# Kernel tuning notes

Measured on AMD Instinct MI355X. Metric: run time of the kernel, lower is better.

## Reference

```python
import jax, jax.numpy as jnp
import numpy as np

NUM_GRAPHS = 256
T, F_IN, F_OUT, D_E = 5, 75, 15, 50   # towers, per-tower in, per-tower out, edge emb dim
N_LAYERS = 4
AVG_DEG_LOG = float(np.log(17.0))     # from deg histogram: all nodes have degree 16 -> mean log(deg+1)=log(17)
BN_EPS = 1e-5
STD_EPS = 1e-5


def _pna_conv(h, src, dst, e_enc, pw, pb, qw, qb, lw, lb):
    """One PNAConv layer (divide_input=False, pre_layers=post_layers=1)."""
    N = h.shape[0]
    x_i, x_j = h[dst], h[src]                      # gather target/source node feats [E, F_IN]
    # pre-NN Linear(3*F_IN -> F_IN) per tower, applied to cat([x_i, x_j, e_enc]); split the weight
    Wi, Wj, We = pw[:, :F_IN], pw[:, F_IN:2 * F_IN], pw[:, 2 * F_IN:]
    m = (jnp.einsum('ef,tfg->etg', x_i, Wi)
         + jnp.einsum('ef,tfg->etg', x_j, Wj)
         + jnp.einsum('ef,tfg->etg', e_enc, We) + pb)   # [E, T, F_IN]
    ones = jnp.ones((m.shape[0],), h.dtype)
    cnt = jax.ops.segment_sum(ones, dst, N)        # in-degree per node
    deg = jnp.maximum(cnt, 1.0)[:, None, None]
    mean = jax.ops.segment_sum(m, dst, N) / deg
    mean2 = jax.ops.segment_sum(m * m, dst, N) / deg
    std = jnp.sqrt(jax.nn.relu(mean2 - mean * mean) + STD_EPS)
    has_edge = (cnt > 0)[:, None, None]
    mn = jnp.where(has_edge, jax.ops.segment_min(m, dst, N), 0.0)
    mx = jnp.where(has_edge, jax.ops.segment_max(m, dst, N), 0.0)
    agg = jnp.concatenate([mean, mn, mx, std], axis=-1)          # [N, T, 4*F_IN]
    amp = (jnp.log(jnp.maximum(cnt, 1.0) + 1.0) / AVG_DEG_LOG)[:, None, None]
    out = jnp.concatenate([agg, agg * amp, agg / amp], axis=-1)  # identity/amplification/attenuation [N,T,12*F_IN]
    post = jnp.einsum('ntf,tfg->ntg', out, qw) + qb              # post-NN Linear(900 -> 15) per tower
    return post.reshape(N, T * F_OUT) @ lw + lb                  # mixing Linear(75 -> 75)


def setup_inputs() -> dict:
    key = jax.random.key(0)
    ks = iter(jax.random.split(key, 64))
    N, E = 16384, 262144
    g = lambda shape, s=0.1: jax.random.normal(next(ks), shape, jnp.float32) * s
    return dict(
        x=jax.random.randint(next(ks), (N,), 0, 21),
        edge_index=jax.random.randint(next(ks), (2, E), 0, N),
        edge_attr=jax.random.randint(next(ks), (E,), 0, 4),
        batch=jnp.sort(jax.random.randint(next(ks), (N,), 0, NUM_GRAPHS)),
        node_emb=g((21, F_IN)),
        edge_emb=g((4, D_E)),
        edge_enc_w=g((N_LAYERS, D_E, F_IN)), edge_enc_b=jnp.zeros((N_LAYERS, F_IN)),
        pre_w=g((N_LAYERS, T, 3 * F_IN, F_IN)), pre_b=jnp.zeros((N_LAYERS, T, F_IN)),
        post_w=g((N_LAYERS, T, 12 * F_IN, F_OUT)), post_b=jnp.zeros((N_LAYERS, T, F_OUT)),
        lin_w=g((N_LAYERS, T * F_OUT, T * F_OUT)), lin_b=jnp.zeros((N_LAYERS, T * F_OUT)),
        bn_gamma=jnp.ones((N_LAYERS, 75)), bn_beta=jnp.zeros((N_LAYERS, 75)),
        mlp_w1=g((75, 50)), mlp_b1=jnp.zeros((50,)),
        mlp_w2=g((50, 25)), mlp_b2=jnp.zeros((25,)),
        mlp_w3=g((25, 1)), mlp_b3=jnp.zeros((1,)),
    )


def reference(x, edge_index, edge_attr, batch, node_emb, edge_emb,
              edge_enc_w, edge_enc_b, pre_w, pre_b, post_w, post_b,
              lin_w, lin_b, bn_gamma, bn_beta,
              mlp_w1, mlp_b1, mlp_w2, mlp_b2, mlp_w3, mlp_b3):
    h = node_emb[x]                    # [N, 75]
    e = edge_emb[edge_attr]            # [E, 50]
    src, dst = edge_index[0], edge_index[1]
    for l in range(N_LAYERS):
        e_enc = e @ edge_enc_w[l] + edge_enc_b[l]   # edge encoder Linear(50->75)
        h = _pna_conv(h, src, dst, e_enc, pre_w[l], pre_b[l],
                      post_w[l], post_b[l], lin_w[l], lin_b[l])
        mu = h.mean(0)
        var = ((h - mu) ** 2).mean(0)               # biased batch-norm variance (training mode)
        h = jax.nn.relu((h - mu) / jnp.sqrt(var + BN_EPS) * bn_gamma[l] + bn_beta[l])
    g = jax.ops.segment_sum(h, batch, NUM_GRAPHS)   # global_add_pool [G, 75]
    g = jax.nn.relu(g @ mlp_w1 + mlp_b1)
    g = jax.nn.relu(g @ mlp_w2 + mlp_b2)
    return g @ mlp_w3 + mlp_b3                      # [G, 1]
```

## Files before the change

### kernel.cpp

```cpp
#include <hip/hip_runtime.h>
#include <math.h>

#define N_NODES 16384
#define N_EDGES 262144
#define TOW 5
#define FI 75
#define FO 15
#define DE 50
#define NL 4
#define NG 256
#define HWP 752
#define AGS 1504
#define PNN 8

static __device__ __attribute__((aligned(16))) float g_hA[N_NODES*FI];
static __device__ __attribute__((aligned(16))) float g_hB[N_NODES*FI];
static __device__ __attribute__((aligned(16))) float g_hW[N_NODES*HWP];
static __device__ __attribute__((aligned(16))) float g_ec[NL*4*376];
static __device__ int   g_deg[N_NODES];
static __device__ int   g_rowstart[N_NODES+1];
static __device__ int   g_cursor[N_NODES];
static __device__ int   g_edge[N_EDGES];
static __device__ float g_mu[FI];
static __device__ float g_rsig[FI];
static __device__ float g_pool[NG*FI];

__global__ void k_embed(const int* __restrict__ x, const float* __restrict__ node_emb) {
    int i = blockIdx.x * blockDim.x + threadIdx.x;
    if (i < N_NODES*FI) {
        int n = i / FI, f = i % FI;
        g_hA[i] = node_emb[x[n]*FI + f];
    }
}

__global__ void k_zerodeg() {
    int i = blockIdx.x * blockDim.x + threadIdx.x;
    if (i < N_NODES) g_deg[i] = 0;
}

__global__ void k_hist(const int* __restrict__ dst) {
    int e = blockIdx.x * blockDim.x + threadIdx.x;
    if (e < N_EDGES) atomicAdd(&g_deg[dst[e]], 1);
}

__global__ void k_scan() {
    __shared__ int part[1024];
    int t = threadIdx.x;
    int base = t * 16;
    int loc[16];
    int s = 0;
    #pragma unroll
    for (int i = 0; i < 16; i++) { loc[i] = s; s += g_deg[base + i]; }
    part[t] = s;
    __syncthreads();
    for (int off = 1; off < 1024; off <<= 1) {
        int v = 0;
        if (t >= off) v = part[t - off];
        __syncthreads();
        if (t >= off) part[t] += v;
        __syncthreads();
    }
    int excl = (t == 0) ? 0 : part[t - 1];
    #pragma unroll
    for (int i = 0; i < 16; i++) {
        g_rowstart[base + i] = excl + loc[i];
        g_cursor[base + i]   = excl + loc[i];
    }
    if (t == 1023) g_rowstart[N_NODES] = part[1023];
}

__global__ void k_scatter(const int* __restrict__ src, const int* __restrict__ dst,
                          const int* __restrict__ attr) {
    int e = blockIdx.x * blockDim.x + threadIdx.x;
    if (e < N_EDGES) {
        int d = dst[e];
        int pos = atomicAdd(&g_cursor[d], 1);
        g_edge[pos] = src[e] | (attr[e] << 16);
    }
}

__global__ void k_ec(const float* __restrict__ edge_emb, const float* __restrict__ edge_enc_w,
                     const float* __restrict__ edge_enc_b, const float* __restrict__ pre_w,
                     const float* __restrict__ pre_b) {
    int l = blockIdx.x;
    const float* eew = edge_enc_w + l*DE*FI;
    const float* eeb = edge_enc_b + l*FI;
    const float* pw  = pre_w + l*TOW*3*FI*FI;
    const float* pb  = pre_b + l*TOW*FI;
    __shared__ float e_enc[4*FI];
    int t = threadIdx.x;
    if (t < 4*FI) {
        int a = t / FI, f = t % FI;
        float s = eeb[f];
        for (int d = 0; d < DE; d++) s += edge_emb[a*DE + d] * eew[d*FI + f];
        e_enc[t] = s;
    }
    __syncthreads();
    for (int o = t; o < 4*376; o += blockDim.x) {
        int a = o / 376;
        int r = o % 376;
        float s = 0.f;
        if (r < TOW*FI) {
            int tw = r / FI, g = r % FI;
            s = pb[tw*FI + g];
            const float* W = pw + (tw*(3*FI) + 2*FI)*FI + g;
            for (int f = 0; f < FI; f++) s += e_enc[a*FI + f] * W[f*FI];
        }
        g_ec[l*1504 + o] = s;
    }
}

#define NPB 8
__global__ void k_hw(const float* __restrict__ pw, const float* __restrict__ gamma,
                     const float* __restrict__ beta, int first) {
    __shared__ float hsh[NPB*FI];
    int n0 = blockIdx.x * NPB;
    int tid = threadIdx.x;
    for (int i = tid; i < NPB*FI; i += blockDim.x) {
        int idx = (n0 + i/FI)*FI + (i % FI);
        float v;
        if (first) {
            v = g_hA[idx];
        } else {
            int c = i % FI;
            v = (g_hB[idx] - g_mu[c]) * g_rsig[c] * gamma[c] + beta[c];
            v = v > 0.f ? v : 0.f;
        }
        hsh[i] = v;
    }
    __syncthreads();
    for (int o = tid; o < 2*TOW*FI; o += blockDim.x) {
        int half = o / (TOW*FI);
        int r = o % (TOW*FI);
        int tw = r / FI, g = r % FI;
        const float* W = pw + (tw*(3*FI) + half*FI)*FI + g;
        float acc[NPB];
        #pragma unroll
        for (int nn = 0; nn < NPB; nn++) acc[nn] = 0.f;
        for (int f = 0; f < FI; f++) {
            float w = W[f*FI];
            #pragma unroll
            for (int nn = 0; nn < NPB; nn++) acc[nn] += hsh[nn*FI + f] * w;
        }
        #pragma unroll
        for (int nn = 0; nn < NPB; nn++)
            g_hW[(n0+nn)*HWP + half*376 + r] = acc[nn];
    }
}

__global__ __launch_bounds__(384) void k_edge(int l, float* __restrict__ agg) {
    __shared__ float aggl[AGS];
    int n = blockIdx.x;
    int tid = threadIdx.x;
    int el = tid & 3;
    int q  = tid >> 2;
    bool act = q < 94;
    const float* ec = g_ec + l*1504;
    int e0 = g_rowstart[n], e1 = g_rowstart[n+1];
    int cnt = e1 - e0;

    if (tid < 4) aggl[1500 + tid] = 0.f;

    float s0=0.f,s1=0.f,s2=0.f,s3=0.f;
    float t0=0.f,t1=0.f,t2=0.f,t3=0.f;
    float mn0=1e30f,mn1=1e30f,mn2=1e30f,mn3=1e30f;
    float mx0=-1e30f,mx1=-1e30f,mx2=-1e30f,mx3=-1e30f;
    float h0=0.f,h1=0.f,h2=0.f,h3=0.f;
    if (act) {
        float4 hv = *(const float4*)&g_hW[n*HWP + 4*q];
        h0=hv.x; h1=hv.y; h2=hv.z; h3=hv.w;
    }

    int nit = (cnt + 15) >> 4;
    for (int it = 0; it < nit; ++it) {
        int ib = e0 + it*16 + el;
        int i0 = ib, i1 = ib+4, i2 = ib+8, i3 = ib+12;
        int pk0 = g_edge[i0 < e1 ? i0 : e0];
        int pk1 = g_edge[i1 < e1 ? i1 : e0];
        int pk2 = g_edge[i2 < e1 ? i2 : e0];
        int pk3 = g_edge[i3 < e1 ? i3 : e0];
        if (act) {
            float4 hj0 = *(const float4*)&g_hW[(pk0 & 0xFFFF)*HWP + 376 + 4*q];
            float4 hj1 = *(const float4*)&g_hW[(pk1 & 0xFFFF)*HWP + 376 + 4*q];
            float4 hj2 = *(const float4*)&g_hW[(pk2 & 0xFFFF)*HWP + 376 + 4*q];
            float4 hj3 = *(const float4*)&g_hW[(pk3 & 0xFFFF)*HWP + 376 + 4*q];
            float4 ev0 = *(const float4*)&ec[(pk0 >> 16)*376 + 4*q];
            float4 ev1 = *(const float4*)&ec[(pk1 >> 16)*376 + 4*q];
            float4 ev2 = *(const float4*)&ec[(pk2 >> 16)*376 + 4*q];
            float4 ev3 = *(const float4*)&ec[(pk3 >> 16)*376 + 4*q];
            #define ACCUM(ii, hj, ev)                                        \
                if (ii < e1) {                                               \
                    float m0 = h0 + hj.x + ev.x;                             \
                    float m1 = h1 + hj.y + ev.y;                             \
                    float m2 = h2 + hj.z + ev.z;                             \
                    float m3 = h3 + hj.w + ev.w;                             \
                    s0 += m0; s1 += m1; s2 += m2; s3 += m3;                  \
                    t0 += m0*m0; t1 += m1*m1; t2 += m2*m2; t3 += m3*m3;      \
                    mn0 = fminf(mn0,m0); mn1 = fminf(mn1,m1);                \
                    mn2 = fminf(mn2,m2); mn3 = fminf(mn3,m3);                \
                    mx0 = fmaxf(mx0,m0); mx1 = fmaxf(mx1,m1);                \
                    mx2 = fmaxf(mx2,m2); mx3 = fmaxf(mx3,m3);                \
                }
            ACCUM(i0, hj0, ev0)
            ACCUM(i1, hj1, ev1)
            ACCUM(i2, hj2, ev2)
            ACCUM(i3, hj3, ev3)
            #undef ACCUM
        }
    }
    #define RSUM(v) v += __shfl_xor(v,1); v += __shfl_xor(v,2);
    #define RMIN(v) v = fminf(v,__shfl_xor(v,1)); v = fminf(v,__shfl_xor(v,2));
    #define RMAX(v) v = fmaxf(v,__shfl_xor(v,1)); v = fmaxf(v,__shfl_xor(v,2));
    RSUM(s0) RSUM(s1) RSUM(s2) RSUM(s3)
    RSUM(t0) RSUM(t1) RSUM(t2) RSUM(t3)
    RMIN(mn0) RMIN(mn1) RMIN(mn2) RMIN(mn3)
    RMAX(mx0) RMAX(mx1) RMAX(mx2) RMAX(mx3)

    if (act && el == 0) {
        float inv = 1.0f / ((cnt > 0) ? (float)cnt : 1.0f);
        float sv[4]  = {s0,s1,s2,s3};
        float tv[4]  = {t0,t1,t2,t3};
        float mnv[4] = {mn0,mn1,mn2,mn3};
        float mxv[4] = {mx0,mx1,mx2,mx3};
        #pragma unroll
        for (int j = 0; j < 4; j++) {
            int c = 4*q + j;
            if (c < TOW*FI) {
                int tw = c / FI, f = c - tw*FI;
                float mean  = sv[j]*inv;
                float mean2 = tv[j]*inv;
                float var = mean2 - mean*mean;
                if (var < 0.f) var = 0.f;
                int b = tw*300 + f;
                aggl[b      ] = mean;
                aggl[b +  75] = (cnt > 0) ? mnv[j] : 0.f;
                aggl[b + 150] = (cnt > 0) ? mxv[j] : 0.f;
                aggl[b + 225] = sqrtf(var + 1e-5f);
            }
        }
    }
    __syncthreads();
    if (tid < 376)
        *(float4*)&agg[(size_t)n*AGS + 4*tid] = *(const float4*)&aggl[4*tid];
}

__global__ __launch_bounds__(384) void
k_post(const float* __restrict__ agg, const float* __restrict__ qw,
       const float* __restrict__ qb, const float* __restrict__ lw,
       const float* __restrict__ lb) {
    __shared__ float part[5*75*9];
    __shared__ float post[PNN][76];
    __shared__ float s_amp[PNN], s_iamp[PNN];
    int tid = threadIdx.x;
    int n0 = blockIdx.x * PNN;

    if (tid < PNN) {
        int cnt = g_rowstart[n0+tid+1] - g_rowstart[n0+tid];
        float deg = (cnt > 0) ? (float)cnt : 1.0f;
        float amp = logf(deg + 1.0f) * (1.0f/2.8332133440562162f);
        s_amp[tid] = amp; s_iamp[tid] = 1.0f/amp;
    }
    __syncthreads();

    int o = tid % 75, p = tid / 75;
    if (tid < 375) {
        int tw = o / FO, g = o % FO;
        const float* W = qw + tw*900*FO + g;
        const float* ab = agg + (size_t)n0*AGS + tw*300 + p*60;
        float a0[PNN], a1[PNN], a2[PNN];
        #pragma unroll
        for (int nn = 0; nn < PNN; nn++) { a0[nn]=0.f; a1[nn]=0.f; a2[nn]=0.f; }
        int f0 = p*60;
        for (int fq = 0; fq < 15; ++fq) {
            int f = f0 + fq*4;
            float w0a = W[(f  )*FO], w0b = W[(f+1)*FO], w0c = W[(f+2)*FO], w0d = W[(f+3)*FO];
            float w1a = W[(300+f)*FO], w1b = W[(301+f)*FO], w1c = W[(302+f)*FO], w1d = W[(303+f)*FO];
            float w2a = W[(600+f)*FO], w2b = W[(601+f)*FO], w2c = W[(602+f)*FO], w2d = W[(603+f)*FO];
            #pragma unroll
            for (int nn = 0; nn < PNN; nn++) {
                float4 av = *(const float4*)&ab[(size_t)nn*AGS + fq*4];
                a0[nn] += av.x*w0a + av.y*w0b + av.z*w0c + av.w*w0d;
                a1[nn] += av.x*w1a + av.y*w1b + av.z*w1c + av.w*w1d;
                a2[nn] += av.x*w2a + av.y*w2b + av.z*w2c + av.w*w2d;
            }
        }
        #pragma unroll
        for (int nn = 0; nn < PNN; nn++)
            part[p*675 + o*9 + nn] = a0[nn] + s_amp[nn]*a1[nn] + s_iamp[nn]*a2[nn];
    }
    __syncthreads();
    if (tid < 75) {
        #pragma unroll
        for (int nn = 0; nn < PNN; nn++) {
            float s = qb[tid];
            #pragma unroll
            for (int p2 = 0; p2 < 5; p2++) s += part[p2*675 + tid*9 + nn];
            post[nn][tid] = s;
        }
    }
    __syncthreads();
    if (tid < 300) {
        int oo = tid % 75, nna = tid / 75;
        #pragma unroll
        for (int h = 0; h < 2; ++h) {
            int nn = nna + 4*h;
            const float* Wl = lw + oo;
            float s = lb[oo];
            for (int f = 0; f < 75; f++) s += post[nn][f] * Wl[f*75];
            g_hB[(n0+nn)*FI + oo] = s;
        }
    }
}

__global__ void k_bnstat() {
    int c = blockIdx.x;
    int t = threadIdx.x;
    double s = 0.0, s2 = 0.0;
    for (int n = t; n < N_NODES; n += 256) {
        float v = g_hB[n*FI + c];
        s += v; s2 += (double)v * v;
    }
    __shared__ double ps[256], ps2[256];
    ps[t] = s; ps2[t] = s2;
    __syncthreads();
    for (int off = 128; off > 0; off >>= 1) {
        if (t < off) { ps[t] += ps[t+off]; ps2[t] += ps2[t+off]; }
        __syncthreads();
    }
    if (t == 0) {
        double mu = ps[0] / N_NODES;
        double var = ps2[0] / N_NODES - mu*mu;
        if (var < 0.0) var = 0.0;
        g_mu[c]   = (float)mu;
        g_rsig[c] = (float)(1.0 / sqrt(var + 1e-5));
    }
}

__global__ void k_poolzero() {
    int i = blockIdx.x * blockDim.x + threadIdx.x;
    if (i < NG*FI) g_pool[i] = 0.f;
}

__global__ void k_pool(const int* __restrict__ batch, const float* __restrict__ gamma,
                       const float* __restrict__ beta) {
    int i = blockIdx.x * blockDim.x + threadIdx.x;
    if (i < N_NODES*FI) {
        int n = i / FI, c = i % FI;
        float v = (g_hB[i] - g_mu[c]) * g_rsig[c] * gamma[c] + beta[c];
        v = v > 0.f ? v : 0.f;
        atomicAdd(&g_pool[batch[n]*FI + c], v);
    }
}

__global__ void k_mlp(const float* __restrict__ w1, const float* __restrict__ b1,
                      const float* __restrict__ w2, const float* __restrict__ b2,
                      const float* __restrict__ w3, const float* __restrict__ b3,
                      float* __restrict__ out) {
    __shared__ float gin[FI], h1[50], h2[25];
    int gi = blockIdx.x;
    int t = threadIdx.x;
    if (t < FI) gin[t] = g_pool[gi*FI + t];
    __syncthreads();
    if (t < 50) {
        float s = b1[t];
        for (int f = 0; f < FI; f++) s += gin[f] * w1[f*50 + t];
        h1[t] = s > 0.f ? s : 0.f;
    }
    __syncthreads();
    if (t < 25) {
        float s = b2[t];
        for (int f = 0; f < 50; f++) s += h1[f] * w2[f*25 + t];
        h2[t] = s > 0.f ? s : 0.f;
    }
    __syncthreads();
    if (t == 0) {
        float s = b3[0];
        for (int f = 0; f < 25; f++) s += h2[f] * w3[f];
        out[gi] = s;
    }
}

extern "C" void kernel_launch(void* const* d_in, const int* in_sizes, int n_in,
                              void* d_out, int out_size, void* d_ws, size_t ws_size,
                              hipStream_t stream) {
    const int*   x          = (const int*)  d_in[0];
    const int*   edge_index = (const int*)  d_in[1];
    const int*   edge_attr  = (const int*)  d_in[2];
    const int*   batch      = (const int*)  d_in[3];
    const float* node_emb   = (const float*)d_in[4];
    const float* edge_emb   = (const float*)d_in[5];
    const float* edge_enc_w = (const float*)d_in[6];
    const float* edge_enc_b = (const float*)d_in[7];
    const float* pre_w      = (const float*)d_in[8];
    const float* pre_b      = (const float*)d_in[9];
    const float* post_w     = (const float*)d_in[10];
    const float* post_b     = (const float*)d_in[11];
    const float* lin_w      = (const float*)d_in[12];
    const float* lin_b      = (const float*)d_in[13];
    const float* bn_gamma   = (const float*)d_in[14];
    const float* bn_beta    = (const float*)d_in[15];
    const float* mlp_w1     = (const float*)d_in[16];
    const float* mlp_b1     = (const float*)d_in[17];
    const float* mlp_w2     = (const float*)d_in[18];
    const float* mlp_b2     = (const float*)d_in[19];
    const float* mlp_w3     = (const float*)d_in[20];
    const float* mlp_b3     = (const float*)d_in[21];
    float* out = (float*)d_out;
    float* agg = (float*)d_ws;

    const int* src = edge_index;
    const int* dst = edge_index + N_EDGES;

    k_embed<<<(N_NODES*FI + 255)/256, 256, 0, stream>>>(x, node_emb);
    k_zerodeg<<<(N_NODES + 255)/256, 256, 0, stream>>>();
    k_hist<<<(N_EDGES + 255)/256, 256, 0, stream>>>(dst);
    k_scan<<<1, 1024, 0, stream>>>();
    k_scatter<<<(N_EDGES + 255)/256, 256, 0, stream>>>(src, dst, edge_attr);
    k_ec<<<NL, 512, 0, stream>>>(edge_emb, edge_enc_w, edge_enc_b, pre_w, pre_b);

    for (int l = 0; l < NL; l++) {
        const float* pw  = pre_w  + l*TOW*(3*FI)*FI;
        const float* qw  = post_w + l*TOW*900*FO;
        const float* qb  = post_b + l*TOW*FO;
        const float* lw  = lin_w  + l*(TOW*FO)*(TOW*FO);
        const float* lb  = lin_b  + l*TOW*FO;
        const float* gamP = bn_gamma + (l > 0 ? (l-1)*FI : 0);
        const float* betP = bn_beta  + (l > 0 ? (l-1)*FI : 0);

        k_hw<<<N_NODES/NPB, 256, 0, stream>>>(pw, gamP, betP, l == 0 ? 1 : 0);
        k_edge<<<N_NODES, 384, 0, stream>>>(l, agg);
        k_post<<<N_NODES/PNN, 384, 0, stream>>>(agg, qw, qb, lw, lb);
        k_bnstat<<<FI, 256, 0, stream>>>();
    }

    k_poolzero<<<(NG*FI + 255)/256, 256, 0, stream>>>();
    k_pool<<<(N_NODES*FI + 255)/256, 256, 0, stream>>>(batch, bn_gamma + 3*FI, bn_beta + 3*FI);
    k_mlp<<<NG, 128, 0, stream>>>(mlp_w1, mlp_b1, mlp_w2, mlp_b2, mlp_w3, mlp_b3, out);
}
```

Measured before the change: 1.349 ms.

## Remap edge aggregation to one thread per feature quad, stage agg in LDS for post

k_edge now processes four nodes per block, with 128 threads per node. Each thread walks all edges of its node for one float4 feature chunk instead of splitting edges across four lanes, which removes the shuffle reductions and the shared-memory staging; results are written directly to global memory with scalar stores. k_post halves nodes per block to 4 and first copies the aggregate rows into shared memory with float4 loads before the weight contraction. The trade-offs are less edge-level parallelism per node, longer serial loops, and uncoalesced scalar global writes.

Result: no change. 1.336 ms (-1.0%).

```diff
diff --git a/kernel.cpp b/kernel.cpp
--- a/kernel.cpp
+++ b/kernel.cpp
@@ -11,7 +11,8 @@
 #define NG 256
 #define HWP 752
 #define AGS 1504
-#define PNN 8
+#define PNN 4
+#define ENB 4
 
 static __device__ __attribute__((aligned(16))) float g_hA[N_NODES*FI];
 static __device__ __attribute__((aligned(16))) float g_hB[N_NODES*FI];
@@ -148,18 +149,15 @@
     }
 }
 
-__global__ __launch_bounds__(384) void k_edge(int l, float* __restrict__ agg) {
-    __shared__ float aggl[AGS];
-    int n = blockIdx.x;
+__global__ __launch_bounds__(128*ENB) void k_edge(int l, float* __restrict__ agg) {
     int tid = threadIdx.x;
-    int el = tid & 3;
-    int q  = tid >> 2;
+    int wp  = tid >> 7;
+    int q   = tid & 127;
+    int n   = blockIdx.x * ENB + wp;
     bool act = q < 94;
     const float* ec = g_ec + l*1504;
     int e0 = g_rowstart[n], e1 = g_rowstart[n+1];
     int cnt = e1 - e0;
-
-    if (tid < 4) aggl[1500 + tid] = 0.f;
 
     float s0=0.f,s1=0.f,s2=0.f,s3=0.f;
     float t0=0.f,t1=0.f,t2=0.f,t3=0.f;
@@ -171,14 +169,12 @@
         h0=hv.x; h1=hv.y; h2=hv.z; h3=hv.w;
     }
 
-    int nit = (cnt + 15) >> 4;
-    for (int it = 0; it < nit; ++it) {
-        int ib = e0 + it*16 + el;
-        int i0 = ib, i1 = ib+4, i2 = ib+8, i3 = ib+12;
-        int pk0 = g_edge[i0 < e1 ? i0 : e0];
-        int pk1 = g_edge[i1 < e1 ? i1 : e0];
-        int pk2 = g_edge[i2 < e1 ? i2 : e0];
-        int pk3 = g_edge[i3 < e1 ? i3 : e0];
+    for (int e = e0; e < e1; e += 4) {
+        int i1 = e+1, i2 = e+2, i3 = e+3;
+        int pk0 = g_edge[e];
+        int pk1 = g_edge[i1 < e1 ? i1 : e];
+        int pk2 = g_edge[i2 < e1 ? i2 : e];
+        int pk3 = g_edge[i3 < e1 ? i3 : e];
         if (act) {
             float4 hj0 = *(const float4*)&g_hW[(pk0 & 0xFFFF)*HWP + 376 + 4*q];
             float4 hj1 = *(const float4*)&g_hW[(pk1 & 0xFFFF)*HWP + 376 + 4*q];
@@ -201,27 +197,21 @@
                     mx0 = fmaxf(mx0,m0); mx1 = fmaxf(mx1,m1);                \
                     mx2 = fmaxf(mx2,m2); mx3 = fmaxf(mx3,m3);                \
                 }
-            ACCUM(i0, hj0, ev0)
+            ACCUM(e,  hj0, ev0)
             ACCUM(i1, hj1, ev1)
             ACCUM(i2, hj2, ev2)
             ACCUM(i3, hj3, ev3)
             #undef ACCUM
         }
     }
-    #define RSUM(v) v += __shfl_xor(v,1); v += __shfl_xor(v,2);
-    #define RMIN(v) v = fminf(v,__shfl_xor(v,1)); v = fminf(v,__shfl_xor(v,2));
-    #define RMAX(v) v = fmaxf(v,__shfl_xor(v,1)); v = fmaxf(v,__shfl_xor(v,2));
-    RSUM(s0) RSUM(s1) RSUM(s2) RSUM(s3)
-    RSUM(t0) RSUM(t1) RSUM(t2) RSUM(t3)
-    RMIN(mn0) RMIN(mn1) RMIN(mn2) RMIN(mn3)
-    RMAX(mx0) RMAX(mx1) RMAX(mx2) RMAX(mx3)
-
-    if (act && el == 0) {
+
+    if (act) {
         float inv = 1.0f / ((cnt > 0) ? (float)cnt : 1.0f);
         float sv[4]  = {s0,s1,s2,s3};
         float tv[4]  = {t0,t1,t2,t3};
         float mnv[4] = {mn0,mn1,mn2,mn3};
         float mxv[4] = {mx0,mx1,mx2,mx3};
+        float* ar = agg + (size_t)n*AGS;
         #pragma unroll
         for (int j = 0; j < 4; j++) {
             int c = 4*q + j;
@@ -232,28 +222,30 @@
                 float var = mean2 - mean*mean;
                 if (var < 0.f) var = 0.f;
                 int b = tw*300 + f;
-                aggl[b      ] = mean;
-                aggl[b +  75] = (cnt > 0) ? mnv[j] : 0.f;
-                aggl[b + 150] = (cnt > 0) ? mxv[j] : 0.f;
-                aggl[b + 225] = sqrtf(var + 1e-5f);
+                ar[b      ] = mean;
+                ar[b +  75] = (cnt > 0) ? mnv[j] : 0.f;
+                ar[b + 150] = (cnt > 0) ? mxv[j] : 0.f;
+                ar[b + 225] = sqrtf(var + 1e-5f);
             }
         }
     }
-    __syncthreads();
-    if (tid < 376)
-        *(float4*)&agg[(size_t)n*AGS + 4*tid] = *(const float4*)&aggl[4*tid];
 }
 
 __global__ __launch_bounds__(384) void
 k_post(const float* __restrict__ agg, const float* __restrict__ qw,
        const float* __restrict__ qb, const float* __restrict__ lw,
        const float* __restrict__ lb) {
-    __shared__ float part[5*75*9];
+    __shared__ __align__(16) float aggs[PNN][AGS];
+    __shared__ float part[5*75*5];
     __shared__ float post[PNN][76];
     __shared__ float s_amp[PNN], s_iamp[PNN];
     int tid = threadIdx.x;
     int n0 = blockIdx.x * PNN;
 
+    for (int i = tid; i < PNN*376; i += 384) {
+        int nn = i / 376, t4 = i % 376;
+        *(float4*)&aggs[nn][4*t4] = *(const float4*)&agg[(size_t)(n0+nn)*AGS + 4*t4];
+    }
     if (tid < PNN) {
         int cnt = g_rowstart[n0+tid+1] - g_rowstart[n0+tid];
         float deg = (cnt > 0) ? (float)cnt : 1.0f;
@@ -266,7 +258,6 @@
     if (tid < 375) {
         int tw = o / FO, g = o % FO;
         const float* W = qw + tw*900*FO + g;
-        const float* ab = agg + (size_t)n0*AGS + tw*300 + p*60;
         float a0[PNN], a1[PNN], a2[PNN];
         #pragma unroll
         for (int nn = 0; nn < PNN; nn++) { a0[nn]=0.f; a1[nn]=0.f; a2[nn]=0.f; }
@@ -278,7 +269,7 @@
             float w2a = W[(600+f)*FO], w2b = W[(601+f)*FO], w2c = W[(602+f)*FO], w2d = W[(603+f)*FO];
             #pragma unroll
             for (int nn = 0; nn < PNN; nn++) {
-                float4 av = *(const float4*)&ab[(size_t)nn*AGS + fq*4];
+                float4 av = *(const float4*)&aggs[nn][tw*300 + f];
                 a0[nn] += av.x*w0a + av.y*w0b + av.z*w0c + av.w*w0d;
                 a1[nn] += av.x*w1a + av.y*w1b + av.z*w1c + av.w*w1d;
                 a2[nn] += av.x*w2a + av.y*w2b + av.z*w2c + av.w*w2d;
@@ -286,7 +277,7 @@
         }
         #pragma unroll
         for (int nn = 0; nn < PNN; nn++)
-            part[p*675 + o*9 + nn] = a0[nn] + s_amp[nn]*a1[nn] + s_iamp[nn]*a2[nn];
+            part[(p*75 + o)*5 + nn] = a0[nn] + s_amp[nn]*a1[nn] + s_iamp[nn]*a2[nn];
     }
     __syncthreads();
     if (tid < 75) {
@@ -294,21 +285,17 @@
         for (int nn = 0; nn < PNN; nn++) {
             float s = qb[tid];
             #pragma unroll
-            for (int p2 = 0; p2 < 5; p2++) s += part[p2*675 + tid*9 + nn];
+            for (int p2 = 0; p2 < 5; p2++) s += part[(p2*75 + tid)*5 + nn];
             post[nn][tid] = s;
         }
     }
     __syncthreads();
     if (tid < 300) {
-        int oo = tid % 75, nna = tid / 75;
-        #pragma unroll
-        for (int h = 0; h < 2; ++h) {
-            int nn = nna + 4*h;
-            const float* Wl = lw + oo;
-            float s = lb[oo];
-            for (int f = 0; f < 75; f++) s += post[nn][f] * Wl[f*75];
-            g_hB[(n0+nn)*FI + oo] = s;
-        }
+        int oo = tid % 75, nn = tid / 75;
+        const float* Wl = lw + oo;
+        float s = lb[oo];
+        for (int f = 0; f < 75; f++) s += post[nn][f] * Wl[f*75];
+        g_hB[(n0+nn)*FI + oo] = s;
     }
 }
 
@@ -428,7 +415,7 @@
         const float* betP = bn_beta  + (l > 0 ? (l-1)*FI : 0);
 
         k_hw<<<N_NODES/NPB, 256, 0, stream>>>(pw, gamP, betP, l == 0 ? 1 : 0);
-        k_edge<<<N_NODES, 384, 0, stream>>>(l, agg);
+        k_edge<<<N_NODES/ENB, 128*ENB, 0, stream>>>(l, agg);
         k_post<<<N_NODES/PNN, 384, 0, stream>>>(agg, qw, qb, lw, lb);
         k_bnstat<<<FI, 256, 0, stream>>>();
     }
```
